# Optimization experiments

Hardware: AMD Instinct MI355X
Metric: run time of the kernel (lower is better)

The kernel has to match this reference:

```python
import jax, jax.numpy as jnp
import numpy as np

NUM_LAYERS = 3

def setup_inputs() -> dict:
    key = jax.random.key(0)
    ku, ki, ke1, ke2 = jax.random.split(key, 4)
    num_users, num_items, D, E = 100000, 50000, 128, 1000000
    # xavier-uniform-ish init scale for the embedding tables
    bound = float(np.sqrt(6.0 / (num_users + D)))
    user_w = jax.random.uniform(ku, (num_users, D), jnp.float32, -bound, bound)
    bound_i = float(np.sqrt(6.0 / (num_items + D)))
    item_w = jax.random.uniform(ki, (num_items, D), jnp.float32, -bound_i, bound_i)
    # bipartite edges: user -> item (item ids offset by num_users), plus reverse direction
    u = jax.random.randint(ke1, (E,), 0, num_users, dtype=jnp.int32)
    v = jax.random.randint(ke2, (E,), 0, num_items, dtype=jnp.int32) + num_users
    edge_index = jnp.stack([jnp.concatenate([u, v]), jnp.concatenate([v, u])])  # [2, 2E]
    return {"user_w": user_w, "item_w": item_w, "edge_index": edge_index,
            "num_users": num_users, "num_items": num_items}

def reference(user_w, item_w, edge_index, num_users, num_items):
    n_nodes = num_users + num_items
    src, dst = edge_index[0], edge_index[1]
    # degree via scatter-add (duplicate edges sum, same as coalesce)
    deg = jax.ops.segment_sum(jnp.ones_like(src, dtype=user_w.dtype), src,
                              num_segments=n_nodes)
    dinv = jnp.where(deg > 0, deg ** -0.5, 0.0)
    dinv = jnp.where(jnp.isfinite(dinv), dinv, 0.0)
    vals = dinv[src] * dinv[dst]  # normalized adjacency values, [2E]

    emb = jnp.concatenate([user_w, item_w], axis=0)  # [n_nodes, D]
    acc = emb
    x = emb
    for _ in range(NUM_LAYERS):
        # SpMM: out[s] += vals(e) * x[dst(e)]
        x = jax.ops.segment_sum(vals[:, None] * x[dst], src, num_segments=n_nodes)
        acc = acc + x
    final = acc / jnp.asarray(NUM_LAYERS + 1, dtype=emb.dtype)
    return final[:num_users], final[num_users:]
```

## Files before the change

### kernel.cpp

```cpp
#include <hip/hip_runtime.h>
#include <hip/hip_fp16.h>
#include <cstdint>
#include <cstddef>

#define D 128
#define BSH 9
#define BNODES 512
#define NBMAX 512
#define CCHUNK 8192
#define CCHUNK_H 2048
#define FP8_SCALE 2048.0f
#define FP8_INV_SCALE (1.0f / 2048.0f)

typedef float v2f __attribute__((ext_vector_type(2)));

static __device__ inline unsigned pack_fp8x4(float a, float b, float c, float d) {
    a = fminf(fmaxf(a, -440.f), 440.f);
    b = fminf(fmaxf(b, -440.f), 440.f);
    c = fminf(fmaxf(c, -440.f), 440.f);
    d = fminf(fmaxf(d, -440.f), 440.f);
    int r = 0;
    r = __builtin_amdgcn_cvt_pk_fp8_f32(a, b, r, false);
    r = __builtin_amdgcn_cvt_pk_fp8_f32(c, d, r, true);
    return (unsigned)r;
}


__global__ __launch_bounds__(256)
void k_hist_tohalf(const int* __restrict__ src, int* __restrict__ bhist,
                   int ne2, int nb, int nbh,
                   const float2* __restrict__ uw, const float2* __restrict__ iw,
                   __half2* __restrict__ x0, int nu2, int ntot2) {
    if ((int)blockIdx.x < nbh) {
        __shared__ int lc[NBMAX];
        for (int i = threadIdx.x; i < nb; i += 256) lc[i] = 0;
        __syncthreads();
        int base = blockIdx.x * CCHUNK_H;
        int lim = min(base + CCHUNK_H, ne2);
        for (int e = base + threadIdx.x; e < lim; e += 256)
            atomicAdd(&lc[src[e] >> BSH], 1);
        __syncthreads();
        for (int i = threadIdx.x; i < nb; i += 256)
            if (lc[i]) atomicAdd(&bhist[i], lc[i]);
    } else {
        int g = (blockIdx.x - nbh) * 256 + threadIdx.x;
        if (g < ntot2) {
            float2 v = (g < nu2) ? uw[g] : iw[g - nu2];
            x0[g] = __floats2half2_rn(v.x, v.y);
        }
    }
}

__global__ void k_bscan(const int* __restrict__ bhist, int* __restrict__ bbase,
                        int* __restrict__ bfill, int* __restrict__ rp,
                        int nb, int nn, int ne2) {
    __shared__ int a[NBMAX], b2[NBMAX];
    int t = threadIdx.x;
    int v = (t < nb) ? bhist[t] : 0;
    a[t] = v;
    __syncthreads();
    int* cur = a; int* nxt = b2;
    for (int o = 1; o < NBMAX; o <<= 1) {
        int x = cur[t];
        if (t >= o) x += cur[t - o];
        nxt[t] = x;
        __syncthreads();
        int* tm = cur; cur = nxt; nxt = tm;
    }
    int excl = cur[t] - v;
    if (t < nb) { bbase[t] = excl; bfill[t] = excl; }
    if (t == 0) { bbase[nb] = ne2; rp[nn] = ne2; }
}

__global__ __launch_bounds__(512)
void k_scatter(const int* __restrict__ src, const int* __restrict__ dst,
               int* __restrict__ bfill, int* __restrict__ tmp, int ne2, int nb) {
    __shared__ int lc[NBMAX], lb[NBMAX];
    for (int i = threadIdx.x; i < nb; i += 512) lc[i] = 0;
    __syncthreads();
    int base = blockIdx.x * CCHUNK;
    int rec[CCHUNK / 512];
#pragma unroll
    for (int i = 0; i < CCHUNK / 512; ++i) {
        int e = base + i * 512 + threadIdx.x;
        rec[i] = -1;
        if (e < ne2) {
            int b = src[e] >> BSH;
            int r = atomicAdd(&lc[b], 1);
            rec[i] = (r << BSH) | b;
        }
    }
    __syncthreads();
    for (int i = threadIdx.x; i < nb; i += 512)
        if (lc[i]) lb[i] = atomicAdd(&bfill[i], lc[i]);
    __syncthreads();
#pragma unroll
    for (int i = 0; i < CCHUNK / 512; ++i) {
        if (rec[i] >= 0) {
            int e = base + i * 512 + threadIdx.x;
            int b = rec[i] & (BNODES - 1);
            int r = rec[i] >> BSH;
            tmp[lb[b] + r] = ((src[e] & (BNODES - 1)) << 18) | dst[e];
        }
    }
}

__global__ __launch_bounds__(512)
void k_build(const int* __restrict__ tmp, const int* __restrict__ bbase,
             int* __restrict__ col, int* __restrict__ rp,
             float* __restrict__ dinv2, float* __restrict__ rinv,
             const float4* __restrict__ x0h, uint2* __restrict__ y0p, int nn) {
    __shared__ int cnt[BNODES];
    __shared__ int off[BNODES];
    __shared__ int wtot[8], woff[8];
    int bkt = blockIdx.x;
    int n0 = bkt << BSH;
    int nloc = min(BNODES, nn - n0);
    int ebeg = bbase[bkt], eend = bbase[bkt + 1];
    int t = threadIdx.x;
    cnt[t] = 0;
    __syncthreads();
    for (int e = ebeg + t; e < eend; e += 512)
        atomicAdd(&cnt[tmp[e] >> 18], 1);
    __syncthreads();
    int v = cnt[t];
    int lane = t & 63, wid = t >> 6;
    int x = v;
#pragma unroll
    for (int o = 1; o < 64; o <<= 1) {
        int y = __shfl_up(x, o);
        if (lane >= o) x += y;
    }
    if (lane == 63) wtot[wid] = x;
    __syncthreads();
    if (t == 0) { int a = 0; for (int k = 0; k < 8; ++k) { woff[k] = a; a += wtot[k]; } }
    __syncthreads();
    off[t] = woff[wid] + x - v;
    __syncthreads();
    if (t < nloc) {
        rp[n0 + t] = ebeg + off[t];
        int c = cnt[t];
        float fc = (float)c;
        dinv2[n0 + t] = (c > 0) ? 1.0f / fc : 0.0f;
        rinv[n0 + t]  = (c > 0) ? sqrtf(fc) : 0.0f;
    }
    {
        int r = t >> 4;
        int l = t & 15;
        for (; r < nloc; r += 32) {
            int c = cnt[r];
            float sc = (c > 0) ? FP8_SCALE * rsqrtf((float)c) : 0.0f;
            float4 fv = x0h[(size_t)(n0 + r) * 16 + l];
            const __half2* hp = reinterpret_cast<const __half2*>(&fv);
            float2 f0 = __half22float2(hp[0]), f1 = __half22float2(hp[1]);
            float2 f2 = __half22float2(hp[2]), f3 = __half22float2(hp[3]);
            uint2 o;
            o.x = pack_fp8x4(sc * f0.x, sc * f0.y, sc * f1.x, sc * f1.y);
            o.y = pack_fp8x4(sc * f2.x, sc * f2.y, sc * f3.x, sc * f3.y);
            y0p[(size_t)(n0 + r) * 16 + l] = o;
        }
    }
    __syncthreads();
    cnt[t] = 0;
    __syncthreads();
    for (int e = ebeg + t; e < eend; e += 512) {
        int pv = tmp[e];
        int sl = pv >> 18;
        int r = atomicAdd(&cnt[sl], 1);
        col[ebeg + off[sl] + r] = pv & 0x3FFFF;
    }
}

template <bool FINAL>
__global__ __launch_bounds__(256)
void k_spmm(const uint2* __restrict__ yin, const float4* __restrict__ win,
            uint2* __restrict__ y8out, float4* __restrict__ wout,
            float4* __restrict__ outp,
            const int* __restrict__ rp, const int* __restrict__ col,
            const float* __restrict__ dinv2, const float* __restrict__ rinv, int nn) {
    int wave = (blockIdx.x * blockDim.x + threadIdx.x) >> 6;
    int lane = threadIdx.x & 63;
    int g = lane >> 4, l16 = lane & 15;
    int node = wave * 4 + g;
    int beg = 0, end = 0;
    if (node < nn) { beg = rp[node]; end = rp[node + 1]; }
    v2f acc[4];
#pragma unroll
    for (int k = 0; k < 4; ++k) acc[k] = (v2f)(0.f);

    int srcl = g << 4;
    for (int base = beg; base < end; base += 16) {
        int p = base + l16;
        int d = (p < end) ? col[p] : 0;
        int m = min(16, end - base);
#pragma unroll 8
        for (int t = 0; t < m; ++t) {
            int dd = __shfl(d, srcl + t);
            uint2 u = yin[(size_t)dd * 16 + l16];
            acc[0] += __builtin_amdgcn_cvt_pk_f32_fp8((int)u.x, false);
            acc[1] += __builtin_amdgcn_cvt_pk_f32_fp8((int)u.x, true);
            acc[2] += __builtin_amdgcn_cvt_pk_f32_fp8((int)u.y, false);
            acc[3] += __builtin_amdgcn_cvt_pk_f32_fp8((int)u.y, true);
        }
    }
    if (node >= nn) return;
    float s2 = dinv2[node];
    float rs = rinv[node] * FP8_INV_SCALE;
    size_t r16 = (size_t)node * 16 + l16;
    float4 wv4 = win[r16];
    const __half2* wp = reinterpret_cast<const __half2*>(&wv4);
    float w[8];
#pragma unroll
    for (int k = 0; k < 4; ++k) {
        float2 fw = __half22float2(wp[k]);
        w[2 * k]     = fw.x + rs * (s2 * acc[k].x);
        w[2 * k + 1] = fw.y + rs * (s2 * acc[k].y);
    }
    if (!FINAL) {
        uint2 o8;
        o8.x = pack_fp8x4(s2 * acc[0].x, s2 * acc[0].y, s2 * acc[1].x, s2 * acc[1].y);
        o8.y = pack_fp8x4(s2 * acc[2].x, s2 * acc[2].y, s2 * acc[3].x, s2 * acc[3].y);
        y8out[r16] = o8;
        __half2 h[4];
#pragma unroll
        for (int k = 0; k < 4; ++k)
            h[k] = __floats2half2_rn(w[2 * k], w[2 * k + 1]);
        wout[r16] = *reinterpret_cast<const float4*>(h);
    } else {
        float4 w0 = make_float4(0.25f * w[0], 0.25f * w[1], 0.25f * w[2], 0.25f * w[3]);
        float4 w1 = make_float4(0.25f * w[4], 0.25f * w[5], 0.25f * w[6], 0.25f * w[7]);
        size_t r32 = (size_t)node * 32 + 2 * l16;
        outp[r32] = w0;
        outp[r32 + 1] = w1;
    }
}


extern "C" void kernel_launch(void* const* d_in, const int* in_sizes, int n_in,
                              void* d_out, int out_size, void* d_ws, size_t ws_size,
                              hipStream_t stream) {
    const float* uw = (const float*)d_in[0];
    const float* iw = (const float*)d_in[1];
    const int* ei = (const int*)d_in[2];

    const int NU = in_sizes[0] / D;
    const int NI = in_sizes[1] / D;
    const int NN = NU + NI;
    const int NE2 = in_sizes[2] / 2;
    const int* src = ei;
    const int* dst = ei + NE2;
    const int NB = (NN + BNODES - 1) >> BSH;

    char* p = (char*)d_ws;
    auto alloc = [&](size_t bytes) -> void* {
        void* r = (void*)p;
        p += (bytes + 255) & ~(size_t)255;
        return r;
    };
    int* bhist   = (int*)alloc(NBMAX * 4);
    int* bbase   = (int*)alloc((NBMAX + 1) * 4);
    int* bfill   = (int*)alloc(NBMAX * 4);
    int* rp      = (int*)alloc((size_t)(NN + 1) * 4);
    float* dinv2 = (float*)alloc((size_t)NN * 4);
    float* rinv  = (float*)alloc((size_t)NN * 4);
    int* col     = (int*)alloc((size_t)NE2 * 4);
    __half2* wh0 = (__half2*)alloc((size_t)NN * D * 2);
    int* tmp     = (int*)wh0;
    __half2* xa  = (__half2*)alloc((size_t)NN * D * 2);
    uint2* y0p   = (uint2*)alloc((size_t)NN * D);
    uint2* y1p   = (uint2*)alloc((size_t)NN * D);
    __half2* wh1 = xa;
    uint2* y2p   = y0p;
    float* outp  = (float*)d_out;

    hipMemsetAsync(bhist, 0, NBMAX * 4, stream);

    int ntot2 = NN * (D / 2);
    int nu2 = NU * (D / 2);
    int nbh = (NE2 + CCHUNK_H - 1) / CCHUNK_H;
    int bi = (ntot2 + 255) / 256;
    int bsc = (NE2 + CCHUNK - 1) / CCHUNK;

    k_hist_tohalf<<<nbh + bi, 256, 0, stream>>>(src, bhist, NE2, NB, nbh,
                                                (const float2*)uw, (const float2*)iw,
                                                xa, nu2, ntot2);
    k_bscan<<<1, NBMAX, 0, stream>>>(bhist, bbase, bfill, rp, NB, NN, NE2);
    k_scatter<<<bsc, 512, 0, stream>>>(src, dst, bfill, tmp, NE2, NB);
    k_build<<<NB, 512, 0, stream>>>(tmp, bbase, col, rp, dinv2, rinv,
                                    (const float4*)xa, y0p, NN);

    int bs = (NN + 15) / 16;
    k_spmm<false><<<bs, 256, 0, stream>>>((const uint2*)y0p, (const float4*)xa,
                                          y1p, (float4*)wh0, nullptr,
                                          rp, col, dinv2, rinv, NN);
    k_spmm<false><<<bs, 256, 0, stream>>>((const uint2*)y1p, (const float4*)wh0,
                                          y2p, (float4*)wh1, nullptr,
                                          rp, col, dinv2, rinv, NN);
    k_spmm<true><<<bs, 256, 0, stream>>>((const uint2*)y2p, (const float4*)wh1,
                                         nullptr, nullptr, (float4*)outp,
                                         rp, col, dinv2, rinv, NN);
}
```

Measured before the change: 383.6 us.

## Drop fp16 staging pass, read fp32 embeddings directly, widen SpMM gathers to 16B

Removes the separate fp32-to-fp16 conversion of the embedding tables. The build kernel and the first SpMM layer now read the fp32 user and item tables directly, which avoids writing and re-reading a full fp16 copy. The SpMM kernel now assigns 8 lanes per node with uint4 (16-byte) fp8 gathers instead of 16 lanes with 8-byte loads, halving the number of gather instructions per neighbor row. The scatter kernel also moves to 256-thread blocks with smaller chunks. In exchange, each lane holds more registers and per-node parallelism is lower.

```diff
diff --git a/kernel.cpp b/kernel.cpp
--- a/kernel.cpp
+++ b/kernel.cpp
@@ -7,7 +7,7 @@
 #define BSH 9
 #define BNODES 512
 #define NBMAX 512
-#define CCHUNK 8192
+#define CCHUNK 4096
 #define CCHUNK_H 2048
 #define FP8_SCALE 2048.0f
 #define FP8_INV_SCALE (1.0f / 2048.0f)
@@ -27,28 +27,17 @@
 
 
 __global__ __launch_bounds__(256)
-void k_hist_tohalf(const int* __restrict__ src, int* __restrict__ bhist,
-                   int ne2, int nb, int nbh,
-                   const float2* __restrict__ uw, const float2* __restrict__ iw,
-                   __half2* __restrict__ x0, int nu2, int ntot2) {
-    if ((int)blockIdx.x < nbh) {
-        __shared__ int lc[NBMAX];
-        for (int i = threadIdx.x; i < nb; i += 256) lc[i] = 0;
-        __syncthreads();
-        int base = blockIdx.x * CCHUNK_H;
-        int lim = min(base + CCHUNK_H, ne2);
-        for (int e = base + threadIdx.x; e < lim; e += 256)
-            atomicAdd(&lc[src[e] >> BSH], 1);
-        __syncthreads();
-        for (int i = threadIdx.x; i < nb; i += 256)
-            if (lc[i]) atomicAdd(&bhist[i], lc[i]);
-    } else {
-        int g = (blockIdx.x - nbh) * 256 + threadIdx.x;
-        if (g < ntot2) {
-            float2 v = (g < nu2) ? uw[g] : iw[g - nu2];
-            x0[g] = __floats2half2_rn(v.x, v.y);
-        }
-    }
+void k_hist(const int* __restrict__ src, int* __restrict__ bhist, int ne2, int nb) {
+    __shared__ int lc[NBMAX];
+    for (int i = threadIdx.x; i < nb; i += 256) lc[i] = 0;
+    __syncthreads();
+    int base = blockIdx.x * CCHUNK_H;
+    int lim = min(base + CCHUNK_H, ne2);
+    for (int e = base + threadIdx.x; e < lim; e += 256)
+        atomicAdd(&lc[src[e] >> BSH], 1);
+    __syncthreads();
+    for (int i = threadIdx.x; i < nb; i += 256)
+        if (lc[i]) atomicAdd(&bhist[i], lc[i]);
 }
 
 __global__ void k_bscan(const int* __restrict__ bhist, int* __restrict__ bbase,
@@ -72,17 +61,17 @@
     if (t == 0) { bbase[nb] = ne2; rp[nn] = ne2; }
 }
 
-__global__ __launch_bounds__(512)
+__global__ __launch_bounds__(256)
 void k_scatter(const int* __restrict__ src, const int* __restrict__ dst,
                int* __restrict__ bfill, int* __restrict__ tmp, int ne2, int nb) {
     __shared__ int lc[NBMAX], lb[NBMAX];
-    for (int i = threadIdx.x; i < nb; i += 512) lc[i] = 0;
+    for (int i = threadIdx.x; i < nb; i += 256) lc[i] = 0;
     __syncthreads();
     int base = blockIdx.x * CCHUNK;
-    int rec[CCHUNK / 512];
-#pragma unroll
-    for (int i = 0; i < CCHUNK / 512; ++i) {
-        int e = base + i * 512 + threadIdx.x;
+    int rec[CCHUNK / 256];
+#pragma unroll
+    for (int i = 0; i < CCHUNK / 256; ++i) {
+        int e = base + i * 256 + threadIdx.x;
         rec[i] = -1;
         if (e < ne2) {
             int b = src[e] >> BSH;
@@ -91,13 +80,13 @@
         }
     }
     __syncthreads();
-    for (int i = threadIdx.x; i < nb; i += 512)
+    for (int i = threadIdx.x; i < nb; i += 256)
         if (lc[i]) lb[i] = atomicAdd(&bfill[i], lc[i]);
     __syncthreads();
 #pragma unroll
-    for (int i = 0; i < CCHUNK / 512; ++i) {
+    for (int i = 0; i < CCHUNK / 256; ++i) {
         if (rec[i] >= 0) {
-            int e = base + i * 512 + threadIdx.x;
+            int e = base + i * 256 + threadIdx.x;
             int b = rec[i] & (BNODES - 1);
             int r = rec[i] >> BSH;
             tmp[lb[b] + r] = ((src[e] & (BNODES - 1)) << 18) | dst[e];
@@ -109,7 +98,8 @@
 void k_build(const int* __restrict__ tmp, const int* __restrict__ bbase,
              int* __restrict__ col, int* __restrict__ rp,
              float* __restrict__ dinv2, float* __restrict__ rinv,
-             const float4* __restrict__ x0h, uint2* __restrict__ y0p, int nn) {
+             const float4* __restrict__ uw, const float4* __restrict__ iw,
+             uint4* __restrict__ y0p, int nu, int nn) {
     __shared__ int cnt[BNODES];
     __shared__ int off[BNODES];
     __shared__ int wtot[8], woff[8];
@@ -145,19 +135,22 @@
         rinv[n0 + t]  = (c > 0) ? sqrtf(fc) : 0.0f;
     }
     {
-        int r = t >> 4;
-        int l = t & 15;
-        for (; r < nloc; r += 32) {
+        int r = t >> 3;
+        int l = t & 7;
+        for (; r < nloc; r += 64) {
+            int gn = n0 + r;
             int c = cnt[r];
             float sc = (c > 0) ? FP8_SCALE * rsqrtf((float)c) : 0.0f;
-            float4 fv = x0h[(size_t)(n0 + r) * 16 + l];
-            const __half2* hp = reinterpret_cast<const __half2*>(&fv);
-            float2 f0 = __half22float2(hp[0]), f1 = __half22float2(hp[1]);
-            float2 f2 = __half22float2(hp[2]), f3 = __half22float2(hp[3]);
-            uint2 o;
-            o.x = pack_fp8x4(sc * f0.x, sc * f0.y, sc * f1.x, sc * f1.y);
-            o.y = pack_fp8x4(sc * f2.x, sc * f2.y, sc * f3.x, sc * f3.y);
-            y0p[(size_t)(n0 + r) * 16 + l] = o;
+            const float4* wb = (gn < nu) ? uw + (size_t)gn * 32
+                                         : iw + (size_t)(gn - nu) * 32;
+            float4 f0 = wb[l * 4 + 0], f1 = wb[l * 4 + 1];
+            float4 f2 = wb[l * 4 + 2], f3 = wb[l * 4 + 3];
+            uint4 o;
+            o.x = pack_fp8x4(sc * f0.x, sc * f0.y, sc * f0.z, sc * f0.w);
+            o.y = pack_fp8x4(sc * f1.x, sc * f1.y, sc * f1.z, sc * f1.w);
+            o.z = pack_fp8x4(sc * f2.x, sc * f2.y, sc * f2.z, sc * f2.w);
+            o.w = pack_fp8x4(sc * f3.x, sc * f3.y, sc * f3.z, sc * f3.w);
+            y0p[(size_t)gn * 8 + l] = o;
         }
     }
     __syncthreads();
@@ -171,67 +164,102 @@
     }
 }
 
-template <bool FINAL>
+template <int MODE>
 __global__ __launch_bounds__(256)
-void k_spmm(const uint2* __restrict__ yin, const float4* __restrict__ win,
-            uint2* __restrict__ y8out, float4* __restrict__ wout,
+void k_spmm(const uint4* __restrict__ yin, const float4* __restrict__ uwf,
+            const float4* __restrict__ iwf, const float4* __restrict__ winh,
+            uint4* __restrict__ y8out, float4* __restrict__ wout,
             float4* __restrict__ outp,
             const int* __restrict__ rp, const int* __restrict__ col,
-            const float* __restrict__ dinv2, const float* __restrict__ rinv, int nn) {
+            const float* __restrict__ dinv2, const float* __restrict__ rinv,
+            int nu, int nn) {
     int wave = (blockIdx.x * blockDim.x + threadIdx.x) >> 6;
     int lane = threadIdx.x & 63;
-    int g = lane >> 4, l16 = lane & 15;
-    int node = wave * 4 + g;
+    int g = lane >> 3, l8 = lane & 7;
+    int node = wave * 8 + g;
     int beg = 0, end = 0;
-    if (node < nn) { beg = rp[node]; end = rp[node + 1]; }
-    v2f acc[4];
-#pragma unroll
-    for (int k = 0; k < 4; ++k) acc[k] = (v2f)(0.f);
-
-    int srcl = g << 4;
-    for (int base = beg; base < end; base += 16) {
-        int p = base + l16;
+    float s2 = 0.f, rv = 0.f;
+    if (node < nn) {
+        beg = rp[node]; end = rp[node + 1];
+        s2 = dinv2[node]; rv = rinv[node];
+    }
+    v2f acc[8];
+#pragma unroll
+    for (int k = 0; k < 8; ++k) acc[k] = (v2f)(0.f);
+
+    int srcl = g << 3;
+    for (int base = beg; base < end; base += 8) {
+        int p = base + l8;
         int d = (p < end) ? col[p] : 0;
-        int m = min(16, end - base);
+        int m = min(8, end - base);
 #pragma unroll 8
         for (int t = 0; t < m; ++t) {
             int dd = __shfl(d, srcl + t);
-            uint2 u = yin[(size_t)dd * 16 + l16];
+            uint4 u = yin[(size_t)dd * 8 + l8];
             acc[0] += __builtin_amdgcn_cvt_pk_f32_fp8((int)u.x, false);
             acc[1] += __builtin_amdgcn_cvt_pk_f32_fp8((int)u.x, true);
             acc[2] += __builtin_amdgcn_cvt_pk_f32_fp8((int)u.y, false);
             acc[3] += __builtin_amdgcn_cvt_pk_f32_fp8((int)u.y, true);
+            acc[4] += __builtin_amdgcn_cvt_pk_f32_fp8((int)u.z, false);
+            acc[5] += __builtin_amdgcn_cvt_pk_f32_fp8((int)u.z, true);
+            acc[6] += __builtin_amdgcn_cvt_pk_f32_fp8((int)u.w, false);
+            acc[7] += __builtin_amdgcn_cvt_pk_f32_fp8((int)u.w, true);
         }
     }
     if (node >= nn) return;
-    float s2 = dinv2[node];
-    float rs = rinv[node] * FP8_INV_SCALE;
-    size_t r16 = (size_t)node * 16 + l16;
-    float4 wv4 = win[r16];
-    const __half2* wp = reinterpret_cast<const __half2*>(&wv4);
-    float w[8];
-#pragma unroll
-    for (int k = 0; k < 4; ++k) {
-        float2 fw = __half22float2(wp[k]);
-        w[2 * k]     = fw.x + rs * (s2 * acc[k].x);
-        w[2 * k + 1] = fw.y + rs * (s2 * acc[k].y);
-    }
-    if (!FINAL) {
-        uint2 o8;
+    float rs = rv * FP8_INV_SCALE;
+    float w[16];
+    if (MODE == 0) {
+        const float4* wb = (node < nu) ? uwf + (size_t)node * 32
+                                       : iwf + (size_t)(node - nu) * 32;
+        float4 f0 = wb[l8 * 4 + 0], f1 = wb[l8 * 4 + 1];
+        float4 f2 = wb[l8 * 4 + 2], f3 = wb[l8 * 4 + 3];
+        w[0]=f0.x; w[1]=f0.y; w[2]=f0.z; w[3]=f0.w;
+        w[4]=f1.x; w[5]=f1.y; w[6]=f1.z; w[7]=f1.w;
+        w[8]=f2.x; w[9]=f2.y; w[10]=f2.z; w[11]=f2.w;
+        w[12]=f3.x; w[13]=f3.y; w[14]=f3.z; w[15]=f3.w;
+    } else {
+        float4 a0 = winh[(size_t)node * 16 + l8 * 2];
+        float4 a1 = winh[(size_t)node * 16 + l8 * 2 + 1];
+        const __half2* p0 = reinterpret_cast<const __half2*>(&a0);
+        const __half2* p1 = reinterpret_cast<const __half2*>(&a1);
+#pragma unroll
+        for (int k = 0; k < 4; ++k) {
+            float2 f = __half22float2(p0[k]);
+            w[2 * k] = f.x; w[2 * k + 1] = f.y;
+        }
+#pragma unroll
+        for (int k = 0; k < 4; ++k) {
+            float2 f = __half22float2(p1[k]);
+            w[8 + 2 * k] = f.x; w[8 + 2 * k + 1] = f.y;
+        }
+    }
+#pragma unroll
+    for (int k = 0; k < 8; ++k) {
+        w[2 * k]     += rs * (s2 * acc[k].x);
+        w[2 * k + 1] += rs * (s2 * acc[k].y);
+    }
+    if (MODE != 2) {
+        uint4 o8;
         o8.x = pack_fp8x4(s2 * acc[0].x, s2 * acc[0].y, s2 * acc[1].x, s2 * acc[1].y);
         o8.y = pack_fp8x4(s2 * acc[2].x, s2 * acc[2].y, s2 * acc[3].x, s2 * acc[3].y);
-        y8out[r16] = o8;
-        __half2 h[4];
-#pragma unroll
-        for (int k = 0; k < 4; ++k)
+        o8.z = pack_fp8x4(s2 * acc[4].x, s2 * acc[4].y, s2 * acc[5].x, s2 * acc[5].y);
+        o8.w = pack_fp8x4(s2 * acc[6].x, s2 * acc[6].y, s2 * acc[7].x, s2 * acc[7].y);
+        y8out[(size_t)node * 8 + l8] = o8;
+        __half2 h[8];
+#pragma unroll
+        for (int k = 0; k < 8; ++k)
             h[k] = __floats2half2_rn(w[2 * k], w[2 * k + 1]);
-        wout[r16] = *reinterpret_cast<const float4*>(h);
+        wout[(size_t)node * 16 + l8 * 2]     = *reinterpret_cast<const float4*>(&h[0]);
+        wout[(size_t)node * 16 + l8 * 2 + 1] = *reinterpret_cast<const float4*>(&h[4]);
     } else {
-        float4 w0 = make_float4(0.25f * w[0], 0.25f * w[1], 0.25f * w[2], 0.25f * w[3]);
-        float4 w1 = make_float4(0.25f * w[4], 0.25f * w[5], 0.25f * w[6], 0.25f * w[7]);
-        size_t r32 = (size_t)node * 32 + 2 * l16;
-        outp[r32] = w0;
-        outp[r32 + 1] = w1;
+        size_t r32 = (size_t)node * 32 + l8 * 4;
+#pragma unroll
+        for (int k = 0; k < 4; ++k) {
+            float4 o = make_float4(0.25f * w[4 * k], 0.25f * w[4 * k + 1],
+                                   0.25f * w[4 * k + 2], 0.25f * w[4 * k + 3]);
+            outp[r32 + k] = o;
+        }
     }
 }
 
@@ -266,37 +294,34 @@
     int* col     = (int*)alloc((size_t)NE2 * 4);
     __half2* wh0 = (__half2*)alloc((size_t)NN * D * 2);
     int* tmp     = (int*)wh0;
-    __half2* xa  = (__half2*)alloc((size_t)NN * D * 2);
-    uint2* y0p   = (uint2*)alloc((size_t)NN * D);
-    uint2* y1p   = (uint2*)alloc((size_t)NN * D);
-    __half2* wh1 = xa;
-    uint2* y2p   = y0p;
+    __half2* wh1 = (__half2*)alloc((size_t)NN * D * 2);
+    uint4* y0p   = (uint4*)alloc((size_t)NN * D);
+    uint4* y1p   = (uint4*)alloc((size_t)NN * D);
+    uint4* y2p   = y0p;
     float* outp  = (float*)d_out;
 
     hipMemsetAsync(bhist, 0, NBMAX * 4, stream);
 
-    int ntot2 = NN * (D / 2);
-    int nu2 = NU * (D / 2);
     int nbh = (NE2 + CCHUNK_H - 1) / CCHUNK_H;
-    int bi = (ntot2 + 255) / 256;
     int bsc = (NE2 + CCHUNK - 1) / CCHUNK;
 
-    k_hist_tohalf<<<nbh + bi, 256, 0, stream>>>(src, bhist, NE2, NB, nbh,
-                                                (const float2*)uw, (const float2*)iw,
-                                                xa, nu2, ntot2);
+    k_hist<<<nbh, 256, 0, stream>>>(src, bhist, NE2, NB);
     k_bscan<<<1, NBMAX, 0, stream>>>(bhist, bbase, bfill, rp, NB, NN, NE2);
-    k_scatter<<<bsc, 512, 0, stream>>>(src, dst, bfill, tmp, NE2, NB);
+    k_scatter<<<bsc, 256, 0, stream>>>(src, dst, bfill, tmp, NE2, NB);
     k_build<<<NB, 512, 0, stream>>>(tmp, bbase, col, rp, dinv2, rinv,
-                                    (const float4*)xa, y0p, NN);
-
-    int bs = (NN + 15) / 16;
-    k_spmm<false><<<bs, 256, 0, stream>>>((const uint2*)y0p, (const float4*)xa,
-                                          y1p, (float4*)wh0, nullptr,
-                                          rp, col, dinv2, rinv, NN);
-    k_spmm<false><<<bs, 256, 0, stream>>>((const uint2*)y1p, (const float4*)wh0,
-                                          y2p, (float4*)wh1, nullptr,
-                                          rp, col, dinv2, rinv, NN);
-    k_spmm<true><<<bs, 256, 0, stream>>>((const uint2*)y2p, (const float4*)wh1,
-                                         nullptr, nullptr, (float4*)outp,
-                                         rp, col, dinv2, rinv, NN);
-}
+                                    (const float4*)uw, (const float4*)iw, y0p, NU, NN);
+
+    int bs = (NN + 31) / 32;
+    k_spmm<0><<<bs, 256, 0, stream>>>((const uint4*)y0p, (const float4*)uw,
+                                      (const float4*)iw, nullptr,
+                                      y1p, (float4*)wh0, nullptr,
+                                      rp, col, dinv2, rinv, NU, NN);
+    k_spmm<1><<<bs, 256, 0, stream>>>((const uint4*)y1p, nullptr, nullptr,
+                                      (const float4*)wh0,
+                                      y2p, (float4*)wh1, nullptr,
+                                      rp, col, dinv2, rinv, NU, NN);
+    k_spmm<2><<<bs, 256, 0, stream>>>((const uint4*)y2p, nullptr, nullptr,
+                                      (const float4*)wh1,
+                                      nullptr, nullptr, (float4*)outp,
+                                      rp, col, dinv2, rinv, NU, NN);
+}
```

Result: no change. 380.6 us (-0.8%).
